# Kernel optimization log

Hardware: AMD Instinct MI355X
Metric: run time of the kernel (lower is better)

The kernel has to match this reference:

```python
import jax, jax.numpy as jnp
import numpy as np

HEAD_DIM = 32
N_HEADS = 4
C = HEAD_DIM * N_HEADS  # 128
N = 256
LN_EPS = 1e-5


def setup_inputs() -> dict:
    key = jax.random.key(0)
    ks = jax.random.split(key, 8)
    s = 1.0 / np.sqrt(C)
    return {
        "x": jax.random.normal(ks[0], (1, N, N, C), dtype=jnp.float32),
        "w_ln": jnp.ones((C,), dtype=jnp.float32),
        "b_ln": jnp.zeros((C,), dtype=jnp.float32),
        "w_b": jax.random.normal(ks[1], (N_HEADS, C), dtype=jnp.float32) * s,
        "w_q": jax.random.normal(ks[2], (C, C), dtype=jnp.float32) * s,
        "w_k": jax.random.normal(ks[3], (C, C), dtype=jnp.float32) * s,
        "w_v": jax.random.normal(ks[4], (C, C), dtype=jnp.float32) * s,
        "w_g": jax.random.normal(ks[5], (C, C), dtype=jnp.float32) * s,
        "w_o": jax.random.normal(ks[6], (C, C), dtype=jnp.float32) * s,
    }


def reference(x, w_ln, b_ln, w_b, w_q, w_k, w_v, w_g, w_o):
    # x: [1, N, N, C]; ending=False -> no permute
    xs = x[0]  # [N, N, C]
    # LayerNorm over last dim
    mu = jnp.mean(xs, axis=-1, keepdims=True)
    var = jnp.mean(jnp.square(xs - mu), axis=-1, keepdims=True)
    h = (xs - mu) * jax.lax.rsqrt(var + LN_EPS) * w_ln + b_ln  # [N, N, C]

    # pair bias: [N, N, h] -> [h, N, N]
    bias = jnp.einsum("ijc,hc->hij", h, w_b)

    # q/k/v: linear (weight stored [out, in], applied as x @ W^T), split heads
    q = jnp.einsum("bkc,oc->bko", h, w_q).reshape(N, N, N_HEADS, HEAD_DIM)
    k = jnp.einsum("bkc,oc->bko", h, w_k).reshape(N, N, N_HEADS, HEAD_DIM)
    v = jnp.einsum("bkc,oc->bko", h, w_v).reshape(N, N, N_HEADS, HEAD_DIM)

    scale = HEAD_DIM ** -0.5
    # scores: [N(b), h, N(q), N(k)], bias broadcast over row-batch b
    a = jnp.einsum("bqhd,bkhd->bhqk", q, k) * scale + bias[None]
    p = jax.nn.softmax(a, axis=-1)
    o = jnp.einsum("bhqk,bkhd->bqhd", p, v).reshape(N, N, C)

    g = jax.nn.sigmoid(jnp.einsum("bkc,oc->bko", h, w_g))
    out = jnp.einsum("bkc,oc->bko", o * g, w_o)  # [N, N, C]
    return out[None]  # [1, N, N, C]
```

## Files before the change

### kernel.cpp

```cpp
#include <hip/hip_runtime.h>

typedef short bf16x8 __attribute__((ext_vector_type(8)));
typedef ushort u16x4 __attribute__((ext_vector_type(4)));
typedef float f32x4 __attribute__((ext_vector_type(4)));

__device__ __forceinline__ ushort f2b(float f) {
    uint u = __builtin_bit_cast(uint, f);
    uint r = (u + 0x7fffu + ((u >> 16) & 1u)) >> 16;
    return (ushort)r;
}
__device__ __forceinline__ float b2f(ushort s) {
    uint u = ((uint)s) << 16;
    return __builtin_bit_cast(float, u);
}
__device__ __forceinline__ uint cvt_pk(float a, float b) {
    uint r;
    asm("v_cvt_pk_bf16_f32 %0, %1, %2" : "=v"(r) : "v"(a), "v"(b));
    return r;
}

__global__ __launch_bounds__(128) void prep_kernel(
        const float* __restrict__ w_q, const float* __restrict__ w_k,
        const float* __restrict__ w_v, const float* __restrict__ w_g,
        const float* __restrict__ w_o,
        ushort* __restrict__ wall, ushort* __restrict__ wo) {
    int row = blockIdx.x, col = threadIdx.x;
    int cs = col ^ ((row & 7) << 3);
    if (row < 512) {
        float val;
        if (row < 128)      val = w_q[row * 128 + col];
        else if (row < 256) val = w_k[(row - 128) * 128 + col];
        else if (row < 384) val = w_v[(row - 256) * 128 + col];
        else                val = w_g[(row - 384) * 128 + col];
        wall[row * 128 + cs] = f2b(val);
    } else {
        int r = row - 512;
        wo[r * 128 + cs] = f2b(w_o[r * 128 + col]);
    }
}

__global__ __launch_bounds__(256, 3) void lnproj_kernel(
        const float* __restrict__ x, const float* __restrict__ w_ln,
        const float* __restrict__ b_ln, const float* __restrict__ w_b,
        const ushort* __restrict__ wall,
        ushort* __restrict__ qp, ushort* __restrict__ kp,
        ushort* __restrict__ vt, ushort* __restrict__ g,
        float* __restrict__ biasT) {
    __shared__ ushort hl[8192];
    __shared__ ushort walls[16384];
    int m0 = blockIdx.x * 64;
    int tid = threadIdx.x, w = tid >> 6, lane = tid & 63;

    for (int idx = tid; idx < 2048; idx += 256)
        ((float4*)walls)[idx] = ((const float4*)wall)[idx];

    {
        int rr = lane >> 2, part = lane & 3;
        int lrow = w * 16 + rr;
        int grow = m0 + lrow;
        const float4* xr = (const float4*)(x + (size_t)grow * 128 + part * 32);
        float4 xv[8];
        float s = 0.f, sq = 0.f;
#pragma unroll
        for (int j = 0; j < 8; ++j) {
            xv[j] = xr[j];
            s += (xv[j].x + xv[j].y) + (xv[j].z + xv[j].w);
            sq += (xv[j].x * xv[j].x + xv[j].y * xv[j].y)
                + (xv[j].z * xv[j].z + xv[j].w * xv[j].w);
        }
        s += __shfl_xor(s, 1);   s += __shfl_xor(s, 2);
        sq += __shfl_xor(sq, 1); sq += __shfl_xor(sq, 2);
        float mean = s * (1.0f / 128.0f);
        float var = sq * (1.0f / 128.0f) - mean * mean;
        float rstd = rsqrtf(var + 1e-5f);
        int c0 = part * 32;
        int swr = (lrow & 7) << 3;
        float pb[4] = {0.f, 0.f, 0.f, 0.f};
#pragma unroll
        for (int j = 0; j < 8; j += 2) {
            ushort hs[8];
#pragma unroll
            for (int jj = 0; jj < 2; ++jj) {
                float4 xj = xv[j + jj];
                float4 wl = ((const float4*)(w_ln + c0))[j + jj];
                float4 bl = ((const float4*)(b_ln + c0))[j + jj];
                float h0 = (xj.x - mean) * rstd * wl.x + bl.x;
                float h1 = (xj.y - mean) * rstd * wl.y + bl.y;
                float h2 = (xj.z - mean) * rstd * wl.z + bl.z;
                float h3 = (xj.w - mean) * rstd * wl.w + bl.w;
#pragma unroll
                for (int hh = 0; hh < 4; ++hh) {
                    float4 wb4 = ((const float4*)(w_b + hh * 128 + c0))[j + jj];
                    pb[hh] += (h0 * wb4.x + h1 * wb4.y) + (h2 * wb4.z + h3 * wb4.w);
                }
                hs[jj * 4 + 0] = f2b(h0); hs[jj * 4 + 1] = f2b(h1);
                hs[jj * 4 + 2] = f2b(h2); hs[jj * 4 + 3] = f2b(h3);
            }
            int col = c0 + j * 4;
            *(bf16x8*)(hl + lrow * 128 + (col ^ swr)) = *(const bf16x8*)hs;
        }
#pragma unroll
        for (int hh = 0; hh < 4; ++hh) {
            pb[hh] += __shfl_xor(pb[hh], 1);
            pb[hh] += __shfl_xor(pb[hh], 2);
        }
        biasT[(size_t)part * 65536 + (size_t)(grow & 255) * 256 + (grow >> 8)] = pb[part];
    }
    __syncthreads();

    int lo = lane & 15, hi = lane >> 4;
    int arow = w * 16 + lo;
    bf16x8 a[4];
#pragma unroll
    for (int ks = 0; ks < 4; ++ks)
        a[ks] = *(const bf16x8*)(hl + arow * 128 +
                                 ((ks * 32 + hi * 8) ^ ((arow & 7) << 3)));
    int bb = m0 >> 8;
    int pcol = (m0 & 255) + w * 16 + lo;
    int pbm = (m0 & 255) + w * 16 + hi * 4;
#pragma unroll 1
    for (int y = 0; y < 4; ++y) {
#pragma unroll
        for (int nt = 0; nt < 8; ++nt) {
            int lr = nt * 16 + lo;
            f32x4 acc = {0.f, 0.f, 0.f, 0.f};
            if (y == 2) {
#pragma unroll
                for (int ks = 0; ks < 4; ++ks) {
                    bf16x8 bf = *(const bf16x8*)(walls + lr * 128 +
                                                 ((ks * 32 + hi * 8) ^ ((lr & 7) << 3)));
                    acc = __builtin_amdgcn_mfma_f32_16x16x32_bf16(a[ks], bf, acc, 0, 0, 0);
                }
                int d = nt * 16 + lo, head = d >> 5, dh = d & 31;
                size_t base = ((size_t)(bb * 4 + head)) * 8192;
                u16x4 t4;
#pragma unroll
                for (int r = 0; r < 4; ++r) t4[r] = f2b(acc[r]);
                *(u16x4*)(vt + base + dh * 256 +
                          ((((pbm >> 3) ^ (dh & 7)) << 3) + (pbm & 7))) = t4;
            } else {
#pragma unroll
                for (int ks = 0; ks < 4; ++ks) {
                    bf16x8 bf = *(const bf16x8*)(walls + lr * 128 +
                                                 ((ks * 32 + hi * 8) ^ ((lr & 7) << 3)));
                    acc = __builtin_amdgcn_mfma_f32_16x16x32_bf16(bf, a[ks], acc, 0, 0, 0);
                }
                if (y == 0) {
                    int head = nt >> 1;
                    size_t base = ((size_t)(bb * 4 + head)) * 8192;
                    u16x4 t4;
#pragma unroll
                    for (int r = 0; r < 4; ++r)
                        t4[r] = f2b(acc[r] * 0.17677669529663687f);
                    *(u16x4*)(qp + base + pcol * 32 + (nt & 1) * 16 + hi * 4) = t4;
                } else if (y == 1) {
                    int head = nt >> 1;
                    size_t base = ((size_t)(bb * 4 + head)) * 8192;
                    int ch = ((nt & 1) * 2 + (hi >> 1)) ^ ((pcol >> 1) & 3);
                    u16x4 t4;
#pragma unroll
                    for (int r = 0; r < 4; ++r) t4[r] = f2b(acc[r]);
                    *(u16x4*)(kp + base + pcol * 32 + ch * 8 + (hi & 1) * 4) = t4;
                } else {
                    u16x4 t4;
#pragma unroll
                    for (int r = 0; r < 4; ++r)
                        t4[r] = f2b(1.0f / (1.0f + __expf(-acc[r])));
                    *(u16x4*)(g + (size_t)(m0 + w * 16 + lo) * 128 +
                              nt * 16 + hi * 4) = t4;
                }
            }
        }
        if (y < 3) {
            __syncthreads();
            for (int idx = tid; idx < 2048; idx += 256)
                ((float4*)walls)[idx] =
                    ((const float4*)(wall + (size_t)(y + 1) * 16384))[idx];
            __syncthreads();
        }
    }
}

__global__ __launch_bounds__(256, 4) void attn_kernel(
        const ushort* __restrict__ qp, const ushort* __restrict__ kp,
        const ushort* __restrict__ vt, const ushort* __restrict__ gm,
        const float* __restrict__ biasT, ushort* __restrict__ og) {
    __shared__ ushort Ks[8192];
    __shared__ ushort Vs[8192];
    __shared__ ushort P[4][1024];
    int blk = blockIdx.x, bh = blk & 1023, hf = blk >> 10;
    int b = bh >> 2, head = bh & 3;
    int tid = threadIdx.x, w = tid >> 6, lane = tid & 63;
    int lo = lane & 15, hi = lane >> 4;
    const ushort* kb = kp + (size_t)bh * 8192;
    const ushort* vb = vt + (size_t)bh * 8192;
    for (int idx = tid; idx < 1024; idx += 256) {
        ((float4*)Ks)[idx] = ((const float4*)kb)[idx];
        ((float4*)Vs)[idx] = ((const float4*)vb)[idx];
    }
    __syncthreads();
    ushort* pw = P[w];
    int vsw = (lo & 7);
    int kch = hi ^ ((lo >> 1) & 3);
    int pw0 = lo * 32 + (((hi >> 1) ^ (lo & 3)) << 3) + ((hi & 1) << 2);
    int pw1 = lo * 32 + (((2 | (hi >> 1)) ^ (lo & 3)) << 3) + ((hi & 1) << 2);
    int prd = lo * 32 + ((hi ^ (lo & 3)) << 3);

    int qrow0 = hf * 128 + w * 32 + lo;
    int qrow1 = qrow0 + 16;
    bf16x8 qa0 = *(const bf16x8*)(qp + (size_t)bh * 8192 + qrow0 * 32 + hi * 8);
    bf16x8 qa1 = *(const bf16x8*)(qp + (size_t)bh * 8192 + qrow1 * 32 + hi * 8);
    const float* btq0 = biasT + (size_t)head * 65536 + (size_t)(hi * 4) * 256 + qrow0;
    const float* btq1 = btq0 + 16;
    float l0 = 0.f, l1 = 0.f;
    f32x4 a00 = {0.f, 0.f, 0.f, 0.f}, a01 = {0.f, 0.f, 0.f, 0.f};
    f32x4 a10 = {0.f, 0.f, 0.f, 0.f}, a11 = {0.f, 0.f, 0.f, 0.f};
#pragma unroll
    for (int c = 0; c < 8; ++c) {
        f32x4 c00, c01, c10, c11;
#pragma unroll
        for (int r = 0; r < 4; ++r) {
            c00[r] = btq0[(c * 32 + r) * 256];
            c01[r] = btq0[(c * 32 + 16 + r) * 256];
            c10[r] = btq1[(c * 32 + r) * 256];
            c11[r] = btq1[(c * 32 + 16 + r) * 256];
        }
        bf16x8 kf0 = *(const bf16x8*)(Ks + (c * 32 + lo) * 32 + kch * 8);
        bf16x8 kf1 = *(const bf16x8*)(Ks + (c * 32 + 16 + lo) * 32 + kch * 8);
        f32x4 s00 = __builtin_amdgcn_mfma_f32_16x16x32_bf16(kf0, qa0, c00, 0, 0, 0);
        f32x4 s01 = __builtin_amdgcn_mfma_f32_16x16x32_bf16(kf1, qa0, c01, 0, 0, 0);
        f32x4 s10 = __builtin_amdgcn_mfma_f32_16x16x32_bf16(kf0, qa1, c10, 0, 0, 0);
        f32x4 s11 = __builtin_amdgcn_mfma_f32_16x16x32_bf16(kf1, qa1, c11, 0, 0, 0);
        float e00 = __expf(s00[0]), e01 = __expf(s00[1]),
              e02 = __expf(s00[2]), e03 = __expf(s00[3]);
        float e04 = __expf(s01[0]), e05 = __expf(s01[1]),
              e06 = __expf(s01[2]), e07 = __expf(s01[3]);
        float e10 = __expf(s10[0]), e11 = __expf(s10[1]),
              e12 = __expf(s10[2]), e13 = __expf(s10[3]);
        float e14 = __expf(s11[0]), e15 = __expf(s11[1]),
              e16 = __expf(s11[2]), e17 = __expf(s11[3]);
        l0 += ((e00 + e01) + (e02 + e03)) + ((e04 + e05) + (e06 + e07));
        l1 += ((e10 + e11) + (e12 + e13)) + ((e14 + e15) + (e16 + e17));
        uint2 w00, w01, w10, w11;
        w00.x = cvt_pk(e00, e01); w00.y = cvt_pk(e02, e03);
        w01.x = cvt_pk(e04, e05); w01.y = cvt_pk(e06, e07);
        w10.x = cvt_pk(e10, e11); w10.y = cvt_pk(e12, e13);
        w11.x = cvt_pk(e14, e15); w11.y = cvt_pk(e16, e17);
        *(uint2*)(pw + pw0) = w00;
        *(uint2*)(pw + pw1) = w01;
        *(uint2*)(pw + 512 + pw0) = w10;
        *(uint2*)(pw + 512 + pw1) = w11;
        bf16x8 pf0 = *(const bf16x8*)(pw + prd);
        bf16x8 pf1 = *(const bf16x8*)(pw + 512 + prd);
        bf16x8 v0 = *(const bf16x8*)(Vs + lo * 256 + (((c * 4 + hi) ^ vsw) << 3));
        bf16x8 v1 = *(const bf16x8*)(Vs + (16 + lo) * 256 + (((c * 4 + hi) ^ vsw) << 3));
        a00 = __builtin_amdgcn_mfma_f32_16x16x32_bf16(v0, pf0, a00, 0, 0, 0);
        a01 = __builtin_amdgcn_mfma_f32_16x16x32_bf16(v1, pf0, a01, 0, 0, 0);
        a10 = __builtin_amdgcn_mfma_f32_16x16x32_bf16(v0, pf1, a10, 0, 0, 0);
        a11 = __builtin_amdgcn_mfma_f32_16x16x32_bf16(v1, pf1, a11, 0, 0, 0);
    }
    l0 += __shfl_xor(l0, 16);
    l0 += __shfl_xor(l0, 32);
    l1 += __shfl_xor(l1, 16);
    l1 += __shfl_xor(l1, 32);
    float rl0 = 1.0f / l0, rl1 = 1.0f / l1;
    int e0 = head * 32 + hi * 4, e1 = e0 + 16;
    int sw = (lo & 7) << 3;
    size_t mr0 = (size_t)b * 256 + qrow0;
    size_t mr1 = mr0 + 16;
    u16x4 g00 = *(const u16x4*)(gm + mr0 * 128 + e0);
    u16x4 g01 = *(const u16x4*)(gm + mr0 * 128 + e1);
    u16x4 g10 = *(const u16x4*)(gm + mr1 * 128 + e0);
    u16x4 g11 = *(const u16x4*)(gm + mr1 * 128 + e1);
    u16x4 o00, o01, o10, o11;
#pragma unroll
    for (int r = 0; r < 4; ++r) {
        o00[r] = f2b(a00[r] * rl0 * b2f(g00[r]));
        o01[r] = f2b(a01[r] * rl0 * b2f(g01[r]));
        o10[r] = f2b(a10[r] * rl1 * b2f(g10[r]));
        o11[r] = f2b(a11[r] * rl1 * b2f(g11[r]));
    }
    *(u16x4*)(og + mr0 * 128 + (e0 ^ sw)) = o00;
    *(u16x4*)(og + mr0 * 128 + (e1 ^ sw)) = o01;
    *(u16x4*)(og + mr1 * 128 + (e0 ^ sw)) = o10;
    *(u16x4*)(og + mr1 * 128 + (e1 ^ sw)) = o11;
}

__global__ __launch_bounds__(256) void out_kernel(
        const ushort* __restrict__ og, const ushort* __restrict__ wo,
        float* __restrict__ out) {
    __shared__ ushort wos[16384];
    int m0 = blockIdx.x * 64;
    for (int idx = threadIdx.x; idx < 2048; idx += 256)
        ((float4*)wos)[idx] = ((const float4*)wo)[idx];
    int tid = threadIdx.x, w = tid >> 6, lane = tid & 63;
    int lo = lane & 15, hi = lane >> 4;
    int arow = m0 + w * 16 + lo;
    bf16x8 oa[4];
#pragma unroll
    for (int ks = 0; ks < 4; ++ks)
        oa[ks] = *(const bf16x8*)(og + (size_t)arow * 128 +
                                  ((ks * 32 + hi * 8) ^ ((arow & 7) << 3)));
    __syncthreads();
    int mrow = m0 + w * 16 + hi * 4;
#pragma unroll
    for (int nt = 0; nt < 8; ++nt) {
        f32x4 acc = {0.f, 0.f, 0.f, 0.f};
        int lr = nt * 16 + lo;
#pragma unroll
        for (int ks = 0; ks < 4; ++ks) {
            bf16x8 bf = *(const bf16x8*)(wos + lr * 128 +
                                         ((ks * 32 + hi * 8) ^ ((lr & 7) << 3)));
            acc = __builtin_amdgcn_mfma_f32_16x16x32_bf16(oa[ks], bf, acc, 0, 0, 0);
        }
#pragma unroll
        for (int r = 0; r < 4; ++r)
            out[(size_t)(mrow + r) * 128 + nt * 16 + lo] = acc[r];
    }
}

extern "C" void kernel_launch(void* const* d_in, const int* in_sizes, int n_in,
                              void* d_out, int out_size, void* d_ws, size_t ws_size,
                              hipStream_t stream) {
    const float* x    = (const float*)d_in[0];
    const float* w_ln = (const float*)d_in[1];
    const float* b_ln = (const float*)d_in[2];
    const float* w_b  = (const float*)d_in[3];
    const float* w_q  = (const float*)d_in[4];
    const float* w_k  = (const float*)d_in[5];
    const float* w_v  = (const float*)d_in[6];
    const float* w_g  = (const float*)d_in[7];
    const float* w_o  = (const float*)d_in[8];
    float* out = (float*)d_out;

    char* ws = (char*)d_ws;
    const size_t MB16 = (size_t)65536 * 128 * sizeof(ushort);
    ushort* qp     = (ushort*)(ws + 0 * MB16);
    ushort* kp     = (ushort*)(ws + 1 * MB16);
    ushort* vt     = (ushort*)(ws + 2 * MB16);
    ushort* g      = (ushort*)(ws + 3 * MB16);
    ushort* og     = (ushort*)(ws + 4 * MB16);
    float*  biasT  = (float*)(ws + 5 * MB16);
    ushort* wall   = (ushort*)(ws + 5 * MB16 + (size_t)65536 * 4 * 4);
    ushort* wo     = wall + 512 * 128;

    prep_kernel<<<640, 128, 0, stream>>>(w_q, w_k, w_v, w_g, w_o, wall, wo);
    lnproj_kernel<<<1024, 256, 0, stream>>>(x, w_ln, b_ln, w_b, wall,
                                            qp, kp, vt, g, biasT);
    attn_kernel<<<2048, 256, 0, stream>>>(qp, kp, vt, g, biasT, og);
    out_kernel<<<1024, 256, 0, stream>>>(og, wo, out);
}
```

Measured before the change: 99.39 us.

## Double-buffer projection weight staging via async global-to-LDS loads

The lnproj kernel now stages projection weights into two 16 KB LDS slots using global_load_lds direct-to-LDS loads. The next slice is prefetched while MFMAs run on the current one, replacing the old synchronous 32 KB reload between projection groups. The LayerNorm output buffer is reused as one of the slots, which lowers LDS usage and lets the launch bound rise from 3 to 5 blocks per CU. Correctness depends on the barriers also waiting for the async LDS loads to complete, and there are now more barrier iterations.

Measured after the change: 96.41 us. 1.03x faster.

```diff
diff --git a/kernel.cpp b/kernel.cpp
--- a/kernel.cpp
+++ b/kernel.cpp
@@ -17,6 +17,17 @@
     uint r;
     asm("v_cvt_pk_bf16_f32 %0, %1, %2" : "=v"(r) : "v"(a), "v"(b));
     return r;
+}
+__device__ __forceinline__ void stage16k(const ushort* gsrc, ushort* ldst,
+                                         int w, int lane) {
+#pragma unroll
+    for (int c2 = 0; c2 < 4; ++c2) {
+        int off = (w * 4 + c2) * 512;
+        __builtin_amdgcn_global_load_lds(
+            (const __attribute__((address_space(1))) void*)(gsrc + off + lane * 8),
+            (__attribute__((address_space(3))) void*)(ldst + off),
+            16, 0, 0);
+    }
 }
 
 __global__ __launch_bounds__(128) void prep_kernel(
@@ -39,20 +50,19 @@
     }
 }
 
-__global__ __launch_bounds__(256, 3) void lnproj_kernel(
+__global__ __launch_bounds__(256, 5) void lnproj_kernel(
         const float* __restrict__ x, const float* __restrict__ w_ln,
         const float* __restrict__ b_ln, const float* __restrict__ w_b,
         const ushort* __restrict__ wall,
         ushort* __restrict__ qp, ushort* __restrict__ kp,
         ushort* __restrict__ vt, ushort* __restrict__ g,
         float* __restrict__ biasT) {
-    __shared__ ushort hl[8192];
-    __shared__ ushort walls[16384];
+    __shared__ ushort slot0[8192];
+    __shared__ ushort slot1[8192];
     int m0 = blockIdx.x * 64;
     int tid = threadIdx.x, w = tid >> 6, lane = tid & 63;
 
-    for (int idx = tid; idx < 2048; idx += 256)
-        ((float4*)walls)[idx] = ((const float4*)wall)[idx];
+    stage16k(wall, slot1, w, lane);
 
     {
         int rr = lane >> 2, part = lane & 3;
@@ -97,7 +107,7 @@
                 hs[jj * 4 + 2] = f2b(h2); hs[jj * 4 + 3] = f2b(h3);
             }
             int col = c0 + j * 4;
-            *(bf16x8*)(hl + lrow * 128 + (col ^ swr)) = *(const bf16x8*)hs;
+            *(bf16x8*)(slot0 + lrow * 128 + (col ^ swr)) = *(const bf16x8*)hs;
         }
 #pragma unroll
         for (int hh = 0; hh < 4; ++hh) {
@@ -113,22 +123,29 @@
     bf16x8 a[4];
 #pragma unroll
     for (int ks = 0; ks < 4; ++ks)
-        a[ks] = *(const bf16x8*)(hl + arow * 128 +
+        a[ks] = *(const bf16x8*)(slot0 + arow * 128 +
                                  ((ks * 32 + hi * 8) ^ ((arow & 7) << 3)));
+    __syncthreads();
+
     int bb = m0 >> 8;
     int pcol = (m0 & 255) + w * 16 + lo;
     int pbm = (m0 & 255) + w * 16 + hi * 4;
 #pragma unroll 1
-    for (int y = 0; y < 4; ++y) {
-#pragma unroll
-        for (int nt = 0; nt < 8; ++nt) {
-            int lr = nt * 16 + lo;
+    for (int s = 0; s < 8; ++s) {
+        if (s < 7)
+            stage16k(wall + (size_t)(s + 1) * 8192, (s & 1) ? slot1 : slot0, w, lane);
+        const ushort* cur = (s & 1) ? slot0 : slot1;
+        int y = s >> 1;
+#pragma unroll
+        for (int ntl = 0; ntl < 4; ++ntl) {
+            int nt = (s & 1) * 4 + ntl;
+            int lrl = ntl * 16 + lo;
             f32x4 acc = {0.f, 0.f, 0.f, 0.f};
             if (y == 2) {
 #pragma unroll
                 for (int ks = 0; ks < 4; ++ks) {
-                    bf16x8 bf = *(const bf16x8*)(walls + lr * 128 +
-                                                 ((ks * 32 + hi * 8) ^ ((lr & 7) << 3)));
+                    bf16x8 bf = *(const bf16x8*)(cur + lrl * 128 +
+                                                 ((ks * 32 + hi * 8) ^ ((lrl & 7) << 3)));
                     acc = __builtin_amdgcn_mfma_f32_16x16x32_bf16(a[ks], bf, acc, 0, 0, 0);
                 }
                 int d = nt * 16 + lo, head = d >> 5, dh = d & 31;
@@ -141,8 +158,8 @@
             } else {
 #pragma unroll
                 for (int ks = 0; ks < 4; ++ks) {
-                    bf16x8 bf = *(const bf16x8*)(walls + lr * 128 +
-                                                 ((ks * 32 + hi * 8) ^ ((lr & 7) << 3)));
+                    bf16x8 bf = *(const bf16x8*)(cur + lrl * 128 +
+                                                 ((ks * 32 + hi * 8) ^ ((lrl & 7) << 3)));
                     acc = __builtin_amdgcn_mfma_f32_16x16x32_bf16(bf, a[ks], acc, 0, 0, 0);
                 }
                 if (y == 0) {
@@ -171,13 +188,7 @@
                 }
             }
         }
-        if (y < 3) {
-            __syncthreads();
-            for (int idx = tid; idx < 2048; idx += 256)
-                ((float4*)walls)[idx] =
-                    ((const float4*)(wall + (size_t)(y + 1) * 16384))[idx];
-            __syncthreads();
-        }
+        __syncthreads();
     }
 }
 
```

## Load projection weights directly from global into registers and add MFMA priority hints

Applied to the files above, without the earlier changes.

The projection kernel no longer stages the fused QKVG weights in shared memory with block-wide barriers between stages. Each wave now loads its B-fragments straight from global memory, relying on L2/L1 caching, in eight half-stages of 64 output rows. This frees 32 KB of LDS and allows occupancy to rise to 4 blocks per CU. The attention kernel also wraps its MFMA groups in s_setprio to favour matrix-instruction issue across waves, at the cost of more global and cache traffic for weights.

New measurement: 107.6 us. 1.08x slower.

```diff
diff --git a/kernel.cpp b/kernel.cpp
--- a/kernel.cpp
+++ b/kernel.cpp
@@ -39,7 +39,7 @@
     }
 }
 
-__global__ __launch_bounds__(256, 3) void lnproj_kernel(
+__global__ __launch_bounds__(256, 4) void lnproj_kernel(
         const float* __restrict__ x, const float* __restrict__ w_ln,
         const float* __restrict__ b_ln, const float* __restrict__ w_b,
         const ushort* __restrict__ wall,
@@ -47,12 +47,8 @@
         ushort* __restrict__ vt, ushort* __restrict__ g,
         float* __restrict__ biasT) {
     __shared__ ushort hl[8192];
-    __shared__ ushort walls[16384];
     int m0 = blockIdx.x * 64;
     int tid = threadIdx.x, w = tid >> 6, lane = tid & 63;
-
-    for (int idx = tid; idx < 2048; idx += 256)
-        ((float4*)walls)[idx] = ((const float4*)wall)[idx];
 
     {
         int rr = lane >> 2, part = lane & 3;
@@ -115,22 +111,31 @@
     for (int ks = 0; ks < 4; ++ks)
         a[ks] = *(const bf16x8*)(hl + arow * 128 +
                                  ((ks * 32 + hi * 8) ^ ((arow & 7) << 3)));
+
     int bb = m0 >> 8;
     int pcol = (m0 & 255) + w * 16 + lo;
     int pbm = (m0 & 255) + w * 16 + hi * 4;
+    int csw = (lo & 7) << 3;
 #pragma unroll 1
-    for (int y = 0; y < 4; ++y) {
-#pragma unroll
-        for (int nt = 0; nt < 8; ++nt) {
-            int lr = nt * 16 + lo;
+    for (int s = 0; s < 8; ++s) {
+        int y = s >> 1;
+        const ushort* wb = wall + (size_t)(y * 128 + (s & 1) * 64) * 128;
+        bf16x8 bfr[4][4];
+#pragma unroll
+        for (int ntl = 0; ntl < 4; ++ntl)
+#pragma unroll
+            for (int ks = 0; ks < 4; ++ks)
+                bfr[ntl][ks] = *(const bf16x8*)(wb + (ntl * 16 + lo) * 128 +
+                                                ((ks * 32 + hi * 8) ^ csw));
+#pragma unroll
+        for (int ntl = 0; ntl < 4; ++ntl) {
+            int nt = (s & 1) * 4 + ntl;
             f32x4 acc = {0.f, 0.f, 0.f, 0.f};
             if (y == 2) {
 #pragma unroll
-                for (int ks = 0; ks < 4; ++ks) {
-                    bf16x8 bf = *(const bf16x8*)(walls + lr * 128 +
-                                                 ((ks * 32 + hi * 8) ^ ((lr & 7) << 3)));
-                    acc = __builtin_amdgcn_mfma_f32_16x16x32_bf16(a[ks], bf, acc, 0, 0, 0);
-                }
+                for (int ks = 0; ks < 4; ++ks)
+                    acc = __builtin_amdgcn_mfma_f32_16x16x32_bf16(a[ks], bfr[ntl][ks],
+                                                                  acc, 0, 0, 0);
                 int d = nt * 16 + lo, head = d >> 5, dh = d & 31;
                 size_t base = ((size_t)(bb * 4 + head)) * 8192;
                 u16x4 t4;
@@ -140,11 +145,9 @@
                           ((((pbm >> 3) ^ (dh & 7)) << 3) + (pbm & 7))) = t4;
             } else {
 #pragma unroll
-                for (int ks = 0; ks < 4; ++ks) {
-                    bf16x8 bf = *(const bf16x8*)(walls + lr * 128 +
-                                                 ((ks * 32 + hi * 8) ^ ((lr & 7) << 3)));
-                    acc = __builtin_amdgcn_mfma_f32_16x16x32_bf16(bf, a[ks], acc, 0, 0, 0);
-                }
+                for (int ks = 0; ks < 4; ++ks)
+                    acc = __builtin_amdgcn_mfma_f32_16x16x32_bf16(bfr[ntl][ks], a[ks],
+                                                                  acc, 0, 0, 0);
                 if (y == 0) {
                     int head = nt >> 1;
                     size_t base = ((size_t)(bb * 4 + head)) * 8192;
@@ -170,13 +173,6 @@
                               nt * 16 + hi * 4) = t4;
                 }
             }
-        }
-        if (y < 3) {
-            __syncthreads();
-            for (int idx = tid; idx < 2048; idx += 256)
-                ((float4*)walls)[idx] =
-                    ((const float4*)(wall + (size_t)(y + 1) * 16384))[idx];
-            __syncthreads();
         }
     }
 }
@@ -227,10 +223,12 @@
         }
         bf16x8 kf0 = *(const bf16x8*)(Ks + (c * 32 + lo) * 32 + kch * 8);
         bf16x8 kf1 = *(const bf16x8*)(Ks + (c * 32 + 16 + lo) * 32 + kch * 8);
+        __builtin_amdgcn_s_setprio(1);
         f32x4 s00 = __builtin_amdgcn_mfma_f32_16x16x32_bf16(kf0, qa0, c00, 0, 0, 0);
         f32x4 s01 = __builtin_amdgcn_mfma_f32_16x16x32_bf16(kf1, qa0, c01, 0, 0, 0);
         f32x4 s10 = __builtin_amdgcn_mfma_f32_16x16x32_bf16(kf0, qa1, c10, 0, 0, 0);
         f32x4 s11 = __builtin_amdgcn_mfma_f32_16x16x32_bf16(kf1, qa1, c11, 0, 0, 0);
+        __builtin_amdgcn_s_setprio(0);
         float e00 = __expf(s00[0]), e01 = __expf(s00[1]),
               e02 = __expf(s00[2]), e03 = __expf(s00[3]);
         float e04 = __expf(s01[0]), e05 = __expf(s01[1]),
@@ -254,10 +252,12 @@
         bf16x8 pf1 = *(const bf16x8*)(pw + 512 + prd);
         bf16x8 v0 = *(const bf16x8*)(Vs + lo * 256 + (((c * 4 + hi) ^ vsw) << 3));
         bf16x8 v1 = *(const bf16x8*)(Vs + (16 + lo) * 256 + (((c * 4 + hi) ^ vsw) << 3));
+        __builtin_amdgcn_s_setprio(1);
         a00 = __builtin_amdgcn_mfma_f32_16x16x32_bf16(v0, pf0, a00, 0, 0, 0);
         a01 = __builtin_amdgcn_mfma_f32_16x16x32_bf16(v1, pf0, a01, 0, 0, 0);
         a10 = __builtin_amdgcn_mfma_f32_16x16x32_bf16(v0, pf1, a10, 0, 0, 0);
         a11 = __builtin_amdgcn_mfma_f32_16x16x32_bf16(v1, pf1, a11, 0, 0, 0);
+        __builtin_amdgcn_s_setprio(0);
     }
     l0 += __shfl_xor(l0, 16);
     l0 += __shfl_xor(l0, 32);
```
